# Kernel optimization log

Hardware: AMD Instinct MI355X
Metric: run time of the kernel (lower is better)

The kernel has to match this reference:

```python
import jax, jax.numpy as jnp
import numpy as np

B, T, C, TH, H, L = 64, 512, 32, 32, 1024, 128


def setup_inputs() -> dict:
    key = jax.random.key(0)
    k1, k2, k3, k4, k5 = jax.random.split(key, 5)
    x = jax.random.normal(k1, (B, T, C), dtype=jnp.float32)
    t = jax.random.uniform(k2, (B, T, TH), dtype=jnp.float32)
    # BasicRNNCell kernel: [(input_dim + hidden), hidden]
    W_rnn = jax.random.normal(k3, (C + TH + H, H), dtype=jnp.float32) * (1.0 / np.sqrt(C + TH + H))
    b_rnn = jnp.zeros((H,), dtype=jnp.float32)
    W_out = jax.random.normal(k4, (H, L), dtype=jnp.float32)
    b_out = jax.random.normal(k5, (L,), dtype=jnp.float32)
    return {"x": x, "t": t, "W_rnn": W_rnn, "b_rnn": b_rnn, "W_out": W_out, "b_out": b_out}


def reference(x, t, W_rnn, b_rnn, W_out, b_out):
    # concat signal and interval features, time-major for scan: [T, B, C+TH]
    seq = jnp.swapaxes(jnp.concatenate([x, t], axis=-1), 0, 1)
    h0 = jnp.zeros((x.shape[0], W_rnn.shape[1]), dtype=x.dtype)

    def step(h, xt):
        # BasicRNNCell: h' = tanh([x_t, h] @ W + b)
        h_new = jnp.tanh(jnp.concatenate([xt, h], axis=-1) @ W_rnn + b_rnn)
        return h_new, None

    h_last, _ = jax.lax.scan(step, h0, seq)
    out = h_last @ W_out + b_out            # [B, L]
    return out[:, None, :]                   # [B, 1, L] (expand_dims axis=1)
```

## Files before the change

kernel.cpp:

```cpp
#include <hip/hip_runtime.h>
#include <math.h>

#define BB   64
#define TT   512
#define CIN  32
#define THF  32
#define HH   1024
#define LL   128
#define INF  64
#define KD   1088
#define KP   1096
#define SR2  1096

typedef short  short8 __attribute__((ext_vector_type(8)));
typedef float  f32x4  __attribute__((ext_vector_type(4)));

static __device__ __forceinline__ unsigned short f2bf(float f) {
    union { float f; unsigned u; } v; v.f = f;
    return (unsigned short)((v.u + 0x7fffu + ((v.u >> 16) & 1u)) >> 16);
}
static __device__ __forceinline__ float bf2f(unsigned short h) {
    union { unsigned u; float f; } v; v.u = ((unsigned)h) << 16;
    return v.f;
}

__global__ __launch_bounds__(256)
void transposeW_bf16(const float* __restrict__ W, unsigned short* __restrict__ Wt) {
    __shared__ float tile[32][33];
    const int ct = blockIdx.x * 32;
    const int kt = blockIdx.y * 32;
    for (int i = threadIdx.y; i < 32; i += 8)
        tile[i][threadIdx.x] = W[(size_t)(kt + i) * HH + ct + threadIdx.x];
    __syncthreads();
    for (int i = threadIdx.y; i < 32; i += 8)
        Wt[(size_t)(ct + i) * KP + kt + threadIdx.x] = f2bf(tile[threadIdx.x][i]);
}

template<int Start, int Count>
static __device__ __forceinline__ f32x4
waveK(const float* __restrict__ x, const float* __restrict__ tfeat,
      const unsigned short* __restrict__ hprev, const short8* __restrict__ brow,
      int b0, int l15, int lg, int t, f32x4 acc)
{
    short8 bf[Count], af[Count];
    #pragma unroll
    for (int i = 0; i < Count; ++i) bf[i] = brow[(Start + i) * 4 + lg];
    #pragma unroll
    for (int i = 0; i < Count; ++i) {
        if (Start + i == 0) {
            const float* xp = &x[((size_t)(b0 + l15) * TT + t) * CIN + lg * 8];
            float4 v0 = *(const float4*)xp, v1 = *(const float4*)(xp + 4);
            short8 a;
            a[0] = (short)f2bf(v0.x); a[1] = (short)f2bf(v0.y);
            a[2] = (short)f2bf(v0.z); a[3] = (short)f2bf(v0.w);
            a[4] = (short)f2bf(v1.x); a[5] = (short)f2bf(v1.y);
            a[6] = (short)f2bf(v1.z); a[7] = (short)f2bf(v1.w);
            af[i] = a;
        } else if (Start + i == 1) {
            const float* tp = &tfeat[((size_t)(b0 + l15) * TT + t) * THF + lg * 8];
            float4 v0 = *(const float4*)tp, v1 = *(const float4*)(tp + 4);
            short8 a;
            a[0] = (short)f2bf(v0.x); a[1] = (short)f2bf(v0.y);
            a[2] = (short)f2bf(v0.z); a[3] = (short)f2bf(v0.w);
            a[4] = (short)f2bf(v1.x); a[5] = (short)f2bf(v1.y);
            a[6] = (short)f2bf(v1.z); a[7] = (short)f2bf(v1.w);
            af[i] = a;
        } else {
            af[i] = ((const short8*)(hprev + (size_t)(b0 + l15) * HH))[(Start + i) * 4 + lg - 8];
        }
    }
    #pragma unroll
    for (int i = 0; i < Count; ++i)
        acc = __builtin_amdgcn_mfma_f32_16x16x32_bf16(af[i], bf[i], acc, 0, 0, 0);
    return acc;
}

__global__ __launch_bounds__(256)
void rnn_step_mfma(const float* __restrict__ x, const float* __restrict__ tfeat,
                   const unsigned short* __restrict__ Wt,
                   const float* __restrict__ bias,
                   const unsigned short* __restrict__ hprev,
                   unsigned short* __restrict__ hnext,
                   int t)
{
    __shared__ float zr[4][16][16];

    const int tid = threadIdx.x;
    const int bid = blockIdx.x;
    const int bg  = bid >> 6, cg = bid & 63;
    const int b0  = bg * 16,  c0 = cg * 16;
    const int w   = tid >> 6, lane = tid & 63;
    const int l15 = lane & 15, lg = lane >> 4;

    const short8* brow = (const short8*)&Wt[(size_t)(c0 + l15) * KP];
    f32x4 acc = {0.f, 0.f, 0.f, 0.f};
    if      (w == 0) acc = waveK< 0, 9>(x, tfeat, hprev, brow, b0, l15, lg, t, acc);
    else if (w == 1) acc = waveK< 9, 9>(x, tfeat, hprev, brow, b0, l15, lg, t, acc);
    else if (w == 2) acc = waveK<18, 8>(x, tfeat, hprev, brow, b0, l15, lg, t, acc);
    else             acc = waveK<26, 8>(x, tfeat, hprev, brow, b0, l15, lg, t, acc);

    #pragma unroll
    for (int r = 0; r < 4; ++r) zr[w][lg * 4 + r][l15] = acc[r];
    __syncthreads();

    {
        int b = tid >> 4, c = tid & 15;
        float z = bias[c0 + c] + zr[0][b][c] + zr[1][b][c] + zr[2][b][c] + zr[3][b][c];
        hnext[(size_t)(b0 + b) * HH + c0 + c] = f2bf(tanhf(z));
    }
}

__global__ __launch_bounds__(128)
void rnn_out_bf16(const unsigned short* __restrict__ h, const float* __restrict__ Wout,
                  const float* __restrict__ bout, float* __restrict__ out)
{
    __shared__ float hl[HH];
    const int b = blockIdx.x, tid = threadIdx.x;
    {
        const short8* hp8 = (const short8*)(h + (size_t)b * HH);
        short8 v = hp8[tid];
        #pragma unroll
        for (int j = 0; j < 8; ++j) hl[tid * 8 + j] = bf2f((unsigned short)v[j]);
    }
    __syncthreads();
    float a0 = bout[tid], a1 = 0.f, a2 = 0.f, a3 = 0.f;
    for (int j = 0; j < HH; j += 4) {
        a0 = fmaf(hl[j + 0], Wout[(size_t)(j + 0) * LL + tid], a0);
        a1 = fmaf(hl[j + 1], Wout[(size_t)(j + 1) * LL + tid], a1);
        a2 = fmaf(hl[j + 2], Wout[(size_t)(j + 2) * LL + tid], a2);
        a3 = fmaf(hl[j + 3], Wout[(size_t)(j + 3) * LL + tid], a3);
    }
    out[(size_t)b * LL + tid] = (a0 + a1) + (a2 + a3);
}

__global__ __launch_bounds__(512, 2)
void rnn_step3(const float* __restrict__ x, const float* __restrict__ tfeat,
               const float* __restrict__ W, const float* __restrict__ bias,
               const float* __restrict__ hprev, float* __restrict__ hnext, int t)
{
    __shared__ float s[16 * SR2];
    __shared__ float zr[8][16][17];
    const int tid = threadIdx.x;
    const int bid = blockIdx.x;
    const int bg = bid >> 6, cg = bid & 63;
    const int b0 = bg * 16, c0 = cg * 16;
    const int q = tid >> 4, bb = (tid >> 2) & 3, cc = tid & 3;
    const int k0 = q * 36;

    const float4* hp4 = reinterpret_cast<const float4*>(hprev) + (size_t)b0 * 256;
    #pragma unroll
    for (int jj = 0; jj < 8; ++jj) {
        int f = tid + 512 * jj;
        int b = f >> 8, c = f & 255;
        float4 v = hp4[f];
        *reinterpret_cast<float4*>(&s[b * SR2 + INF + 4 * c]) = v;
    }
    if (tid < 256) {
        int b = tid >> 4, jf = tid & 15;
        float4 v;
        if (jf < 8) v = *reinterpret_cast<const float4*>(&x[((size_t)(b0 + b) * TT + t) * CIN + jf * 4]);
        else        v = *reinterpret_cast<const float4*>(&tfeat[((size_t)(b0 + b) * TT + t) * THF + (jf - 8) * 4]);
        *reinterpret_cast<float4*>(&s[b * SR2 + jf * 4]) = v;
    }
    __syncthreads();

    int nj = 0;
    if (k0 < KD) { int rem = KD - k0; nj = (rem >= 36) ? 9 : (rem >> 2); }
    const float* wp = W + (size_t)k0 * HH + c0 + 4 * cc;
    const float* sp = s + k0;
    float4 acc0 = {0,0,0,0}, acc1 = {0,0,0,0}, acc2 = {0,0,0,0}, acc3 = {0,0,0,0};
#define FMA4(A, sv, wv) \
    A.x = fmaf(sv, wv.x, A.x); A.y = fmaf(sv, wv.y, A.y); \
    A.z = fmaf(sv, wv.z, A.z); A.w = fmaf(sv, wv.w, A.w);
    #pragma unroll 2
    for (int j = 0; j < nj; ++j) {
        float4 w0 = *reinterpret_cast<const float4*>(wp + (size_t)(4 * j + 0) * HH);
        float4 w1 = *reinterpret_cast<const float4*>(wp + (size_t)(4 * j + 1) * HH);
        float4 w2 = *reinterpret_cast<const float4*>(wp + (size_t)(4 * j + 2) * HH);
        float4 w3 = *reinterpret_cast<const float4*>(wp + (size_t)(4 * j + 3) * HH);
        float4 s0 = *reinterpret_cast<const float4*>(sp + (bb +  0) * SR2 + 4 * j);
        float4 s1 = *reinterpret_cast<const float4*>(sp + (bb +  4) * SR2 + 4 * j);
        float4 s2 = *reinterpret_cast<const float4*>(sp + (bb +  8) * SR2 + 4 * j);
        float4 s3 = *reinterpret_cast<const float4*>(sp + (bb + 12) * SR2 + 4 * j);
        FMA4(acc0, s0.x, w0) FMA4(acc0, s0.y, w1) FMA4(acc0, s0.z, w2) FMA4(acc0, s0.w, w3)
        FMA4(acc1, s1.x, w0) FMA4(acc1, s1.y, w1) FMA4(acc1, s1.z, w2) FMA4(acc1, s1.w, w3)
        FMA4(acc2, s2.x, w0) FMA4(acc2, s2.y, w1) FMA4(acc2, s2.z, w2) FMA4(acc2, s2.w, w3)
        FMA4(acc3, s3.x, w0) FMA4(acc3, s3.y, w1) FMA4(acc3, s3.z, w2) FMA4(acc3, s3.w, w3)
    }
#undef FMA4
#define REDSTEP(A, D) \
    A.x += __shfl_xor(A.x, D); A.y += __shfl_xor(A.y, D); \
    A.z += __shfl_xor(A.z, D); A.w += __shfl_xor(A.w, D);
    REDSTEP(acc0, 16) REDSTEP(acc1, 16) REDSTEP(acc2, 16) REDSTEP(acc3, 16)
    REDSTEP(acc0, 32) REDSTEP(acc1, 32) REDSTEP(acc2, 32) REDSTEP(acc3, 32)
#undef REDSTEP
    if ((tid & 48) == 0) {
        int ww = tid >> 6;
        zr[ww][bb +  0][4*cc+0] = acc0.x; zr[ww][bb +  0][4*cc+1] = acc0.y;
        zr[ww][bb +  0][4*cc+2] = acc0.z; zr[ww][bb +  0][4*cc+3] = acc0.w;
        zr[ww][bb +  4][4*cc+0] = acc1.x; zr[ww][bb +  4][4*cc+1] = acc1.y;
        zr[ww][bb +  4][4*cc+2] = acc1.z; zr[ww][bb +  4][4*cc+3] = acc1.w;
        zr[ww][bb +  8][4*cc+0] = acc2.x; zr[ww][bb +  8][4*cc+1] = acc2.y;
        zr[ww][bb +  8][4*cc+2] = acc2.z; zr[ww][bb +  8][4*cc+3] = acc2.w;
        zr[ww][bb + 12][4*cc+0] = acc3.x; zr[ww][bb + 12][4*cc+1] = acc3.y;
        zr[ww][bb + 12][4*cc+2] = acc3.z; zr[ww][bb + 12][4*cc+3] = acc3.w;
    }
    __syncthreads();
    if (tid < 256) {
        int b = tid >> 4, c = tid & 15;
        float z = bias[c0 + c];
        #pragma unroll
        for (int g = 0; g < 8; ++g) z += zr[g][b][c];
        hnext[(size_t)(b0 + b) * HH + c0 + c] = tanhf(z);
    }
}

__global__ __launch_bounds__(128)
void rnn_out(const float* __restrict__ h, const float* __restrict__ Wout,
             const float* __restrict__ bout, float* __restrict__ out)
{
    __shared__ float hl[HH];
    const int b = blockIdx.x, tid = threadIdx.x;
    for (int i = tid; i < HH / 4; i += 128)
        *reinterpret_cast<float4*>(hl + 4 * i) =
            *reinterpret_cast<const float4*>(h + (size_t)b * HH + 4 * i);
    __syncthreads();
    float a0 = bout[tid], a1 = 0.f, a2 = 0.f, a3 = 0.f;
    for (int j = 0; j < HH; j += 4) {
        a0 = fmaf(hl[j + 0], Wout[(size_t)(j + 0) * LL + tid], a0);
        a1 = fmaf(hl[j + 1], Wout[(size_t)(j + 1) * LL + tid], a1);
        a2 = fmaf(hl[j + 2], Wout[(size_t)(j + 2) * LL + tid], a2);
        a3 = fmaf(hl[j + 3], Wout[(size_t)(j + 3) * LL + tid], a3);
    }
    out[(size_t)b * LL + tid] = (a0 + a1) + (a2 + a3);
}

__global__ __launch_bounds__(512)
void rnn_scan_kernel(const float* __restrict__ x, const float* __restrict__ tf,
                     const float* __restrict__ W, const float* __restrict__ bias,
                     const float* __restrict__ Wout, const float* __restrict__ bout,
                     float* __restrict__ out)
{
    __shared__ float s[KD];
    const int b_idx = blockIdx.x, tid = threadIdx.x;
    if (tid < CIN)      s[tid] = x[b_idx * TT * CIN + tid];
    else if (tid < INF) s[tid] = tf[b_idx * TT * THF + (tid - CIN)];
    for (int i = tid; i < HH; i += 512) s[INF + i] = 0.0f;
    __syncthreads();
    const int j0 = tid * 2;
    const float bias0 = bias[j0], bias1 = bias[j0 + 1];
    for (int t = 0; t < TT; ++t) {
        float z0 = bias0, z1 = bias1;
        #pragma unroll 8
        for (int k = 0; k < KD; ++k) {
            const float2 wv = *reinterpret_cast<const float2*>(&W[(size_t)k * HH + j0]);
            const float sv = s[k];
            z0 = fmaf(sv, wv.x, z0);
            z1 = fmaf(sv, wv.y, z1);
        }
        float nin = 0.0f;
        const int tn = t + 1;
        if (tn < TT) {
            if (tid < CIN)      nin = x[b_idx * TT * CIN + tn * CIN + tid];
            else if (tid < INF) nin = tf[b_idx * TT * THF + tn * THF + (tid - CIN)];
        }
        __syncthreads();
        s[INF + j0]     = tanhf(z0);
        s[INF + j0 + 1] = tanhf(z1);
        if (tid < INF && tn < TT) s[tid] = nin;
        __syncthreads();
    }
    for (int lll = tid; lll < LL; lll += 512) {
        float acc = bout[lll];
        for (int j = 0; j < HH; ++j) acc = fmaf(s[INF + j], Wout[(size_t)j * LL + lll], acc);
        out[(size_t)b_idx * LL + lll] = acc;
    }
}

extern "C" void kernel_launch(void* const* d_in, const int* in_sizes, int n_in,
                              void* d_out, int out_size, void* d_ws, size_t ws_size,
                              hipStream_t stream) {
    const float* x    = (const float*)d_in[0];
    const float* tf   = (const float*)d_in[1];
    const float* W    = (const float*)d_in[2];
    const float* brnn = (const float*)d_in[3];
    const float* Wout = (const float*)d_in[4];
    const float* bout = (const float*)d_in[5];
    float* out = (float*)d_out;

    const size_t hbf_bytes = 2ull * BB * HH * sizeof(unsigned short);
    const size_t wt_bytes  = (size_t)HH * KP * sizeof(unsigned short);
    if (ws_size >= hbf_bytes + wt_bytes) {
        unsigned short* hbf = (unsigned short*)d_ws;
        unsigned short* Wt  = hbf + 2ull * BB * HH;
        hipMemsetAsync(hbf, 0, (size_t)BB * HH * sizeof(unsigned short), stream);
        transposeW_bf16<<<dim3(HH / 32, KD / 32), dim3(32, 8), 0, stream>>>(W, Wt);
        for (int t = 0; t < TT; ++t) {
            rnn_step_mfma<<<256, 256, 0, stream>>>(x, tf, Wt, brnn,
                hbf + (size_t)(t & 1) * BB * HH,
                hbf + (size_t)((t + 1) & 1) * BB * HH, t);
        }
        rnn_out_bf16<<<BB, 128, 0, stream>>>(hbf , Wout, bout, out);
        return;
    }

    float* hbuf = (float*)d_ws;
    const size_t hbuf_bytes = 2ull * BB * HH * sizeof(float);
    if (ws_size < hbuf_bytes) {
        rnn_scan_kernel<<<BB, 512, 0, stream>>>(x, tf, W, brnn, Wout, bout, out);
        return;
    }
    hipMemsetAsync(hbuf, 0, (size_t)BB * HH * sizeof(float), stream);
    for (int t = 0; t < TT; ++t) {
        rnn_step3<<<256, 512, 0, stream>>>(x, tf, W, brnn,
                                           hbuf + (size_t)(t & 1) * BB * HH,
                                           hbuf + (size_t)((t + 1) & 1) * BB * HH,
                                           t);
    }
    rnn_out<<<BB, 128, 0, stream>>>(hbuf, Wout, bout, out);
}
```

Baseline: 1.883 ms.

## Use single-wave blocks per tile, dropping the split-K reduction through shared memory

The per-step RNN kernel now runs one 64-lane wave per 16x16 output tile and walks the full K dimension itself with two interleaved MFMA accumulators. Previously four waves split K and reduced their partial sums through shared memory with a barrier. This removes the LDS reduction and the sync, but each wave now issues four times as many dependent MFMAs and loads, and each block has less parallelism to hide latency.

Result: slower. 2.972 ms (+57.9%).

```diff
diff --git a/kernel.cpp b/kernel.cpp
--- a/kernel.cpp
+++ b/kernel.cpp
@@ -36,77 +36,59 @@
         Wt[(size_t)(ct + i) * KP + kt + threadIdx.x] = f2bf(tile[threadIdx.x][i]);
 }
 
-template<int Start, int Count>
-static __device__ __forceinline__ f32x4
-waveK(const float* __restrict__ x, const float* __restrict__ tfeat,
-      const unsigned short* __restrict__ hprev, const short8* __restrict__ brow,
-      int b0, int l15, int lg, int t, f32x4 acc)
-{
-    short8 bf[Count], af[Count];
-    #pragma unroll
-    for (int i = 0; i < Count; ++i) bf[i] = brow[(Start + i) * 4 + lg];
-    #pragma unroll
-    for (int i = 0; i < Count; ++i) {
-        if (Start + i == 0) {
-            const float* xp = &x[((size_t)(b0 + l15) * TT + t) * CIN + lg * 8];
-            float4 v0 = *(const float4*)xp, v1 = *(const float4*)(xp + 4);
-            short8 a;
-            a[0] = (short)f2bf(v0.x); a[1] = (short)f2bf(v0.y);
-            a[2] = (short)f2bf(v0.z); a[3] = (short)f2bf(v0.w);
-            a[4] = (short)f2bf(v1.x); a[5] = (short)f2bf(v1.y);
-            a[6] = (short)f2bf(v1.z); a[7] = (short)f2bf(v1.w);
-            af[i] = a;
-        } else if (Start + i == 1) {
-            const float* tp = &tfeat[((size_t)(b0 + l15) * TT + t) * THF + lg * 8];
-            float4 v0 = *(const float4*)tp, v1 = *(const float4*)(tp + 4);
-            short8 a;
-            a[0] = (short)f2bf(v0.x); a[1] = (short)f2bf(v0.y);
-            a[2] = (short)f2bf(v0.z); a[3] = (short)f2bf(v0.w);
-            a[4] = (short)f2bf(v1.x); a[5] = (short)f2bf(v1.y);
-            a[6] = (short)f2bf(v1.z); a[7] = (short)f2bf(v1.w);
-            af[i] = a;
-        } else {
-            af[i] = ((const short8*)(hprev + (size_t)(b0 + l15) * HH))[(Start + i) * 4 + lg - 8];
-        }
-    }
-    #pragma unroll
-    for (int i = 0; i < Count; ++i)
-        acc = __builtin_amdgcn_mfma_f32_16x16x32_bf16(af[i], bf[i], acc, 0, 0, 0);
-    return acc;
-}
-
-__global__ __launch_bounds__(256)
-void rnn_step_mfma(const float* __restrict__ x, const float* __restrict__ tfeat,
-                   const unsigned short* __restrict__ Wt,
-                   const float* __restrict__ bias,
-                   const unsigned short* __restrict__ hprev,
-                   unsigned short* __restrict__ hnext,
-                   int t)
-{
-    __shared__ float zr[4][16][16];
-
-    const int tid = threadIdx.x;
+__global__ __launch_bounds__(64)
+void rnn_step4(const float* __restrict__ x, const float* __restrict__ tfeat,
+               const unsigned short* __restrict__ Wt,
+               const float* __restrict__ bias,
+               const unsigned short* __restrict__ hprev,
+               unsigned short* __restrict__ hnext,
+               int t)
+{
     const int bid = blockIdx.x;
     const int bg  = bid >> 6, cg = bid & 63;
     const int b0  = bg * 16,  c0 = cg * 16;
-    const int w   = tid >> 6, lane = tid & 63;
+    const int lane = threadIdx.x;
     const int l15 = lane & 15, lg = lane >> 4;
 
     const short8* brow = (const short8*)&Wt[(size_t)(c0 + l15) * KP];
-    f32x4 acc = {0.f, 0.f, 0.f, 0.f};
-    if      (w == 0) acc = waveK< 0, 9>(x, tfeat, hprev, brow, b0, l15, lg, t, acc);
-    else if (w == 1) acc = waveK< 9, 9>(x, tfeat, hprev, brow, b0, l15, lg, t, acc);
-    else if (w == 2) acc = waveK<18, 8>(x, tfeat, hprev, brow, b0, l15, lg, t, acc);
-    else             acc = waveK<26, 8>(x, tfeat, hprev, brow, b0, l15, lg, t, acc);
-
+    const short8* arow = (const short8*)(hprev + (size_t)(b0 + l15) * HH);
+
+    f32x4 accA = {0.f, 0.f, 0.f, 0.f};
+    f32x4 accB = {0.f, 0.f, 0.f, 0.f};
+
+    {
+        const float* xp = &x[((size_t)(b0 + l15) * TT + t) * CIN + lg * 8];
+        float4 v0 = *(const float4*)xp, v1 = *(const float4*)(xp + 4);
+        short8 a;
+        a[0] = (short)f2bf(v0.x); a[1] = (short)f2bf(v0.y);
+        a[2] = (short)f2bf(v0.z); a[3] = (short)f2bf(v0.w);
+        a[4] = (short)f2bf(v1.x); a[5] = (short)f2bf(v1.y);
+        a[6] = (short)f2bf(v1.z); a[7] = (short)f2bf(v1.w);
+        accA = __builtin_amdgcn_mfma_f32_16x16x32_bf16(a, brow[0 * 4 + lg], accA, 0, 0, 0);
+    }
+    {
+        const float* tp = &tfeat[((size_t)(b0 + l15) * TT + t) * THF + lg * 8];
+        float4 v0 = *(const float4*)tp, v1 = *(const float4*)(tp + 4);
+        short8 a;
+        a[0] = (short)f2bf(v0.x); a[1] = (short)f2bf(v0.y);
+        a[2] = (short)f2bf(v0.z); a[3] = (short)f2bf(v0.w);
+        a[4] = (short)f2bf(v1.x); a[5] = (short)f2bf(v1.y);
+        a[6] = (short)f2bf(v1.z); a[7] = (short)f2bf(v1.w);
+        accB = __builtin_amdgcn_mfma_f32_16x16x32_bf16(a, brow[1 * 4 + lg], accB, 0, 0, 0);
+    }
+    #pragma unroll 4
+    for (int i = 2; i < 34; i += 2) {
+        accA = __builtin_amdgcn_mfma_f32_16x16x32_bf16(
+                   arow[(i - 2) * 4 + lg], brow[i * 4 + lg], accA, 0, 0, 0);
+        accB = __builtin_amdgcn_mfma_f32_16x16x32_bf16(
+                   arow[(i - 1) * 4 + lg], brow[(i + 1) * 4 + lg], accB, 0, 0, 0);
+    }
+
+    const float bn = bias[c0 + l15];
     #pragma unroll
-    for (int r = 0; r < 4; ++r) zr[w][lg * 4 + r][l15] = acc[r];
-    __syncthreads();
-
-    {
-        int b = tid >> 4, c = tid & 15;
-        float z = bias[c0 + c] + zr[0][b][c] + zr[1][b][c] + zr[2][b][c] + zr[3][b][c];
-        hnext[(size_t)(b0 + b) * HH + c0 + c] = f2bf(tanhf(z));
+    for (int r = 0; r < 4; ++r) {
+        float z = accA[r] + accB[r] + bn;
+        hnext[(size_t)(b0 + lg * 4 + r) * HH + c0 + l15] = f2bf(tanhf(z));
     }
 }
 
@@ -296,7 +278,7 @@
         hipMemsetAsync(hbf, 0, (size_t)BB * HH * sizeof(unsigned short), stream);
         transposeW_bf16<<<dim3(HH / 32, KD / 32), dim3(32, 8), 0, stream>>>(W, Wt);
         for (int t = 0; t < TT; ++t) {
-            rnn_step_mfma<<<256, 256, 0, stream>>>(x, tf, Wt, brnn,
+            rnn_step4<<<256, 64, 0, stream>>>(x, tf, Wt, brnn,
                 hbf + (size_t)(t & 1) * BB * HH,
                 hbf + (size_t)((t + 1) & 1) * BB * HH, t);
         }
```
